# Kernel optimization log

Measured on AMD Instinct MI355X. Metric: run time of the kernel, lower is better.

Reference implementation:

```python
import jax, jax.numpy as jnp
import numpy as np

# fixed 9 neighborhood offsets (center + 8 directions), in pixel units
BASE = np.array([[0,0],[-1,-1],[0,-1],[1,-1],[-1,0],[1,0],[-1,1],[0,1],[1,1]], dtype=np.float32)
MAX_DELTA = 0.5 / 512.0


def bilinear_sample(vm, gx, gy):
    """vm: (D,H,W); gx,gy: (N,) normalized grid coords in [-1,1].
    Bilinear, padding_mode='zeros', align_corners=True. Returns (D,N)."""
    D, H, W = vm.shape
    ix = (gx + 1.0) * 0.5 * (W - 1)
    iy = (gy + 1.0) * 0.5 * (H - 1)
    x0 = jnp.floor(ix); y0 = jnp.floor(iy)
    x1 = x0 + 1.0;      y1 = y0 + 1.0
    wx1 = ix - x0; wx0 = 1.0 - wx1
    wy1 = iy - y0; wy0 = 1.0 - wy1
    fm = vm.reshape(D, H * W)

    def corner(xf, yf, wx, wy):
        valid = (xf >= 0) & (xf <= W - 1) & (yf >= 0) & (yf <= H - 1)
        xi = jnp.clip(xf.astype(jnp.int32), 0, W - 1)
        yi = jnp.clip(yf.astype(jnp.int32), 0, H - 1)
        v = jnp.take(fm, yi * W + xi, axis=1)  # (D,N) gather
        w = jnp.where(valid, wx * wy, 0.0)
        return v * w

    return (corner(x0, y0, wx0, wy0) + corner(x1, y0, wx1, wy0)
            + corner(x0, y1, wx0, wy1) + corner(x1, y1, wx1, wy1))


def setup_inputs() -> dict:
    key = jax.random.key(0)
    ks = jax.random.split(key, 5)
    B, C, Hf, Wf = 4, 256, 128, 128
    T, D = 16384, 128
    fmap = jax.random.normal(ks[0], (B, C, Hf, Wf), dtype=jnp.float32)
    coords = jax.random.uniform(ks[1], (B, T, 2), dtype=jnp.float32)
    W_proj = jax.random.normal(ks[2], (D, C), dtype=jnp.float32) * (1.0 / np.sqrt(C))
    W1 = jax.random.normal(ks[3], (D, D), dtype=jnp.float32) * (1.0 / np.sqrt(D))
    b1 = jnp.zeros((D,), dtype=jnp.float32)
    W2 = jax.random.normal(ks[4], (2, D), dtype=jnp.float32) * (1.0 / np.sqrt(D))
    b2 = jnp.zeros((2,), dtype=jnp.float32)
    return {"fmap": fmap, "coords": coords, "W_proj": W_proj,
            "W1": W1, "b1": b1, "W2": W2, "b2": b2}


def reference(fmap, coords, W_proj, W1, b1, W2, b2):
    B, C, Hf, Wf = fmap.shape
    T = coords.shape[1]
    K = BASE.shape[0]
    # 1x1 conv projection
    vm = jnp.einsum('bchw,dc->bdhw', fmap, W_proj)  # (B,D,Hf,Wf)
    # offsets: one pixel step in [0,1] coords (align_corners=True)
    step = jnp.array([1.0 / (Wf - 1), 1.0 / (Hf - 1)], dtype=coords.dtype)
    grid = coords[:, :, None, :] + jnp.asarray(BASE)[None, None] * step  # (B,T,K,2)
    grid = grid * 2.0 - 1.0                                            # normalize to [-1,1]
    grid = grid.reshape(B, T * K, 2)
    feat = jax.vmap(bilinear_sample)(vm, grid[..., 0], grid[..., 1])   # (B,D,T*K)
    D = feat.shape[1]
    feat = feat.transpose(0, 2, 1).reshape(B, T, K, D).mean(axis=2)    # (B,T,D)
    h = jax.nn.relu(feat @ W1.T + b1)
    delta = jnp.tanh(h @ W2.T + b2) * MAX_DELTA
    return coords + delta
```

## Files before the change

kernel.cpp:

```cpp
#include <hip/hip_runtime.h>
#include <cstddef>

#define NB 4
#define NC 256
#define ND 128
#define NH 128
#define NW 128
#define NHW (NH*NW)
#define NT 16384
#define NBKT 1024
#define CAP 192
#define FS 136
#define GGRID 3072
#define CSTRIDE 16

typedef short   short8  __attribute__((ext_vector_type(8)));
typedef unsigned short ushort8 __attribute__((ext_vector_type(8)));
typedef float   floatx4 __attribute__((ext_vector_type(4)));
typedef float   floatx2 __attribute__((ext_vector_type(2)));

__device__ __forceinline__ unsigned pk_bf16(float a, float b) {
    unsigned ua = __float_as_uint(a);
    unsigned ub = __float_as_uint(b);
    ua += 0x7fffu + ((ua >> 16) & 1u);
    ub += 0x7fffu + ((ub >> 16) & 1u);
    return (ua >> 16) | (ub & 0xffff0000u);
}

__device__ __forceinline__ unsigned fp8x4_from_f32(float v0, float v1, float v2, float v3) {
    int r = 0;
    r = __builtin_amdgcn_cvt_pk_fp8_f32(v0, v1, r, false);
    r = __builtin_amdgcn_cvt_pk_fp8_f32(v2, v3, r, true);
    return (unsigned)r;
}
template <bool HI>
__device__ __forceinline__ floatx2 fp8x2_to_f32(unsigned w) {
    return __builtin_amdgcn_cvt_pk_f32_fp8((int)w, HI);
}

__device__ __forceinline__ int bucket_of(float cx, float cy, int b) {
    int x0 = (int)floorf(cx * (float)(NW - 1));
    int y0 = (int)floorf(cy * (float)(NH - 1));
    x0 = min(max(x0, 0), NW - 1);
    y0 = min(max(y0, 0), NH - 1);
    return b * 256 + (y0 >> 3) * 16 + (x0 >> 3);
}

__global__ __launch_bounds__(512, 4)
void proj_fused(const float* __restrict__ fmap, const float* __restrict__ coords,
                const float* __restrict__ Wp, const float* __restrict__ W1,
                int* __restrict__ counts, int* __restrict__ order,
                unsigned short* __restrict__ W1bf, unsigned char* __restrict__ vm)
{
    const int bi = blockIdx.x;
    const int t  = threadIdx.x;

    if (t < 128) {
        const int g = bi * 128 + t;
        const float cx = coords[(size_t)g*2 + 0];
        const float cy = coords[(size_t)g*2 + 1];
        const int bkt = bucket_of(cx, cy, g >> 14);
        const int pos = atomicAdd(&counts[bkt*CSTRIDE], 1);
        if (pos < CAP) order[bkt*CAP + pos] = g;
    } else if (t < 160) {
        const int i = bi * 32 + (t - 128);
        unsigned u = __float_as_uint(W1[i]);
        u += 0x7fffu + ((u >> 16) & 1u);
        W1bf[i] = (unsigned short)(u >> 16);
    }

    __shared__ unsigned short awp[8*8*64*8];
    __shared__ float ftile[32*128];

    const int lane = t & 63;
    const int w    = t >> 6;
    const int l15  = lane & 15;
    const int q    = lane >> 4;
    const int cq   = q * 8;

    {
        const int dt = w;
        const float* wr0 = Wp + (size_t)(dt*16 + l15)*NC + cq;
        #pragma unroll
        for (int ch = 0; ch < 8; ++ch) {
            float4 g0 = *(const float4*)(wr0 + ch*32);
            float4 g1 = *(const float4*)(wr0 + ch*32 + 4);
            uint4 pk = make_uint4(pk_bf16(g0.x,g0.y), pk_bf16(g0.z,g0.w),
                                  pk_bf16(g1.x,g1.y), pk_bf16(g1.z,g1.w));
            *(uint4*)&awp[((dt*8 + ch)*64 + lane)*8] = pk;
        }
    }

    const int b    = (bi & 7) >> 1;
    const int slot = ((bi >> 3) << 1) | (bi & 1);
    const int pl   = w*16 + l15;

    const int row_thr = t >> 5;
    const int px_off  = (t & 31) * 4;
    const float* gstage = fmap + (size_t)b*NC*NHW + slot*128 + px_off;
    char* ftile_b = (char*)ftile;
    const unsigned wbase = (unsigned)((t >> 6) * 1024);

    floatx4 acc[8];
    #pragma unroll
    for (int i = 0; i < 8; ++i) acc[i] = (floatx4)(0.f);

    #pragma unroll 1
    for (int c0 = 0; c0 < 8; ++c0) {
        __syncthreads();
        {
            const float* g0 = gstage + (size_t)(c0*32 + row_thr)*NHW;
            const float* g1 = g0 + (size_t)16*NHW;
            __builtin_amdgcn_global_load_lds(
                (const __attribute__((address_space(1))) unsigned*)g0,
                (__attribute__((address_space(3))) unsigned*)(ftile_b + wbase), 16, 0, 0);
            __builtin_amdgcn_global_load_lds(
                (const __attribute__((address_space(1))) unsigned*)g1,
                (__attribute__((address_space(3))) unsigned*)(ftile_b + 8192 + wbase), 16, 0, 0);
        }
        __syncthreads();

        union { short8 v; unsigned u[4]; } bc;
        #pragma unroll
        for (int j = 0; j < 4; ++j)
            bc.u[j] = pk_bf16(ftile[(cq + 2*j    )*128 + pl],
                              ftile[(cq + 2*j + 1)*128 + pl]);
        #pragma unroll
        for (int dt = 0; dt < 8; ++dt) {
            short8 afr = *(const short8*)&awp[((dt*8 + c0)*64 + lane)*8];
            acc[dt] = __builtin_amdgcn_mfma_f32_16x16x32_bf16(afr, bc.v, acc[dt], 0, 0, 0);
        }
    }

    __syncthreads();
    {
        unsigned* lw = (unsigned*)ftile;
        const int sw = (pl & 7) << 2;
        #pragma unroll
        for (int dt = 0; dt < 8; ++dt) {
            floatx4 v = acc[dt];
            lw[pl*32 + ((dt*4 + q) ^ sw)] = fp8x4_from_f32(v[0], v[1], v[2], v[3]);
        }
    }
    __syncthreads();
    {
        unsigned char* vmbase = vm + ((size_t)(b*NHW + slot*128))*ND;
        const unsigned* lr = (const unsigned*)ftile;
        #pragma unroll
        for (int k = 0; k < 2; ++k) {
            const int px  = (t >> 3) + k*64;
            const int w8b = (t & 7) * 4;
            uint4 vv = *(const uint4*)&lr[px*32 + (w8b ^ ((px & 7) << 2))];
            *(uint4*)(vmbase + k*8192 + t*16) = vv;
        }
    }
}

__global__ __launch_bounds__(512, 4)
void gather_mlp(const unsigned char* __restrict__ vm, const float* __restrict__ coords,
                const int* __restrict__ counts, const int* __restrict__ order,
                const unsigned short* __restrict__ W1bf, const float* __restrict__ b1,
                const float* __restrict__ W2, const float* __restrict__ b2,
                float* __restrict__ out)
{
    __shared__ unsigned short feat[64 * FS];
    __shared__ float part[64][8];
    __shared__ float W2s[256];
    __shared__ float b1s[128];
    __shared__ int gidx[64];

    const int bkt = blockIdx.x & 1023;
    const int c   = blockIdx.x >> 10;
    const int n   = min(counts[bkt*CSTRIDE], CAP);
    const int np  = min(n - c*64, 64);
    if (np <= 0) return;
    const int t   = threadIdx.x;

    if (t < 128) {
        W2s[t*2]   = W2[t];
        W2s[t*2+1] = W2[ND + t];
        b1s[t]     = b1[t];
    }

    {
        const int pt = t >> 3;
        const int c8 = t & 7;
        if (pt < np) {
            const int g = order[bkt*CAP + c*64 + pt];
            if (c8 == 0) gidx[pt] = g;
            const int b = g >> 14;
            const float cx = coords[(size_t)g*2 + 0];
            const float cy = coords[(size_t)g*2 + 1];
            const float ix = cx * (float)(NW - 1);
            const float iy = cy * (float)(NH - 1);
            const float x0f = floorf(ix), y0f = floorf(iy);
            const int x0 = (int)x0f, y0 = (int)y0f;
            const float wx1 = ix - x0f, wy1 = iy - y0f;
            const float wxv[4] = {1.f - wx1, 1.f, 1.f, wx1};
            const float wyv[4] = {1.f - wy1, 1.f, 1.f, wy1};
            floatx2 acc[8];
            #pragma unroll
            for (int k = 0; k < 8; ++k) acc[k] = (floatx2)(0.f);
            const unsigned char* vmb = vm + (size_t)b*NHW*ND + c8*16;
            #pragma unroll
            for (int j = 0; j < 4; ++j) {
                const int Y  = y0 - 1 + j;
                const int Yc = min(max(Y, 0), NH-1);
                const bool vy = (Y >= 0) & (Y < NH);
                #pragma unroll
                for (int i = 0; i < 4; ++i) {
                    const int X  = x0 - 1 + i;
                    const int Xc = min(max(X, 0), NW-1);
                    const bool vx = (X >= 0) & (X < NW);
                    const float wgt = (vx & vy) ? wxv[i]*wyv[j] : 0.f;
                    uint4 u = *(const uint4*)(vmb + (size_t)(Yc*NW + Xc)*ND);
                    const floatx2 w2 = {wgt, wgt};
                    acc[0] += w2 * fp8x2_to_f32<false>(u.x);
                    acc[1] += w2 * fp8x2_to_f32<true >(u.x);
                    acc[2] += w2 * fp8x2_to_f32<false>(u.y);
                    acc[3] += w2 * fp8x2_to_f32<true >(u.y);
                    acc[4] += w2 * fp8x2_to_f32<false>(u.z);
                    acc[5] += w2 * fp8x2_to_f32<true >(u.z);
                    acc[6] += w2 * fp8x2_to_f32<false>(u.w);
                    acc[7] += w2 * fp8x2_to_f32<true >(u.w);
                }
            }
            const float s9 = 1.f/9.f;
            unsigned pk[8];
            #pragma unroll
            for (int k = 0; k < 8; ++k)
                pk[k] = pk_bf16(acc[k].x*s9, acc[k].y*s9);
            *(uint4*)&feat[pt*FS + c8*16]     = make_uint4(pk[0],pk[1],pk[2],pk[3]);
            *(uint4*)&feat[pt*FS + c8*16 + 8] = make_uint4(pk[4],pk[5],pk[6],pk[7]);
        }
    }
    __syncthreads();

    {
        const int lane = t & 63;
        const int w    = t >> 6;
        const int l15  = lane & 15;
        const int q    = lane >> 4;
        const int mp   = w & 3;
        const int npr  = w >> 2;

        if (npr*32 < np) {
            floatx4 C[2][2];
            #pragma unroll
            for (int mi = 0; mi < 2; ++mi)
                #pragma unroll
                for (int ni = 0; ni < 2; ++ni) C[mi][ni] = (floatx4)(0.f);

            #pragma unroll
            for (int kk = 0; kk < 4; ++kk) {
                short8 a0 = *(const short8*)&W1bf[((mp*2+0)*16 + l15)*ND + kk*32 + q*8];
                short8 a1 = *(const short8*)&W1bf[((mp*2+1)*16 + l15)*ND + kk*32 + q*8];
                short8 f0 = *(const short8*)&feat[((npr*2+0)*16 + l15)*FS + kk*32 + q*8];
                short8 f1 = *(const short8*)&feat[((npr*2+1)*16 + l15)*FS + kk*32 + q*8];
                C[0][0] = __builtin_amdgcn_mfma_f32_16x16x32_bf16(a0, f0, C[0][0], 0, 0, 0);
                C[0][1] = __builtin_amdgcn_mfma_f32_16x16x32_bf16(a0, f1, C[0][1], 0, 0, 0);
                C[1][0] = __builtin_amdgcn_mfma_f32_16x16x32_bf16(a1, f0, C[1][0], 0, 0, 0);
                C[1][1] = __builtin_amdgcn_mfma_f32_16x16x32_bf16(a1, f1, C[1][1], 0, 0, 0);
            }
            #pragma unroll
            for (int ni = 0; ni < 2; ++ni) {
                float s0 = 0.f, s1 = 0.f;
                #pragma unroll
                for (int mi = 0; mi < 2; ++mi) {
                    const int e0 = (mp*2 + mi)*16 + q*4;
                    float4 bq = *(const float4*)&b1s[e0];
                    floatx4 h4 = C[mi][ni];
                    #pragma unroll
                    for (int r = 0; r < 4; ++r) {
                        float hv = fmaxf(h4[r] + (&bq.x)[r], 0.f);
                        float2 wv = *(const float2*)&W2s[(e0 + r)*2];
                        s0 = fmaf(hv, wv.x, s0);
                        s1 = fmaf(hv, wv.y, s1);
                    }
                }
                s0 += __shfl_xor(s0, 16); s0 += __shfl_xor(s0, 32);
                s1 += __shfl_xor(s1, 16); s1 += __shfl_xor(s1, 32);
                if (q == 0) {
                    const int pt = (npr*2 + ni)*16 + l15;
                    part[pt][mp*2 + 0] = s0;
                    part[pt][mp*2 + 1] = s1;
                }
            }
        }
    }
    __syncthreads();

    if (t < np) {
        const int g = gidx[t];
        float s0 = part[t][0] + part[t][2] + part[t][4] + part[t][6];
        float s1 = part[t][1] + part[t][3] + part[t][5] + part[t][7];
        const float cx = coords[(size_t)g*2 + 0];
        const float cy = coords[(size_t)g*2 + 1];
        const float MD = 0.5f / 512.0f;
        float2 o = make_float2(cx + tanhf(s0 + b2[0]) * MD,
                               cy + tanhf(s1 + b2[1]) * MD);
        *(float2*)&out[(size_t)g*2] = o;
    }
}

extern "C" void kernel_launch(void* const* d_in, const int* in_sizes, int n_in,
                              void* d_out, int out_size, void* d_ws, size_t ws_size,
                              hipStream_t stream)
{
    const float* fmap   = (const float*)d_in[0];
    const float* coords = (const float*)d_in[1];
    const float* Wp     = (const float*)d_in[2];
    const float* W1     = (const float*)d_in[3];
    const float* b1     = (const float*)d_in[4];
    const float* W2     = (const float*)d_in[5];
    const float* b2     = (const float*)d_in[6];
    float* out = (float*)d_out;

    unsigned char* vm = (unsigned char*)d_ws;
    char* base = (char*)d_ws + (size_t)NB*NHW*ND;
    unsigned short* W1bf = (unsigned short*)base;
    int* counts = (int*)(base + 32768);
    int* order  = (int*)(base + 32768 + 65536);

    hipMemsetAsync(counts, 0, NBKT*CSTRIDE*sizeof(int), stream);
    proj_fused<<<dim3(512),   512, 0, stream>>>(fmap, coords, Wp, W1,
                                                counts, order, W1bf, vm);
    gather_mlp<<<dim3(GGRID), 512, 0, stream>>>(vm, coords, counts, order,
                                                W1bf, b1, W2, b2, out);
}
```

Measured before the change: 135.8 us.

## Double-buffer fmap tile loads into LDS in projection kernel

Splits the fmap staging tile into two LDS buffers and prefetches the next channel chunk with global_load_lds while the MFMA work runs on the current one. Explicit vmcnt waits and raw s_barrier calls replace the two __syncthreads per iteration, and the channel loop is fully unrolled. The goal is to hide global load latency in the projection. In exchange LDS use doubles and launch_bounds drops from 4 to 2 blocks per CU, which may reduce occupancy. The hand-written waitcnt and barrier placement carries ordering risk around the wait for the current buffer, especially for the prologue's waves.

```diff
diff --git a/kernel.cpp b/kernel.cpp
--- a/kernel.cpp
+++ b/kernel.cpp
@@ -46,7 +46,7 @@
     return b * 256 + (y0 >> 3) * 16 + (x0 >> 3);
 }
 
-__global__ __launch_bounds__(512, 4)
+__global__ __launch_bounds__(512, 2)
 void proj_fused(const float* __restrict__ fmap, const float* __restrict__ coords,
                 const float* __restrict__ Wp, const float* __restrict__ W1,
                 int* __restrict__ counts, int* __restrict__ order,
@@ -70,7 +70,7 @@
     }
 
     __shared__ unsigned short awp[8*8*64*8];
-    __shared__ float ftile[32*128];
+    __shared__ float ftile[2][32*128];
 
     const int lane = t & 63;
     const int w    = t >> 6;
@@ -105,34 +105,51 @@
     #pragma unroll
     for (int i = 0; i < 8; ++i) acc[i] = (floatx4)(0.f);
 
-    #pragma unroll 1
+    __syncthreads();
+
+    {
+        const float* g0 = gstage + (size_t)(0*32 + row_thr)*NHW;
+        __builtin_amdgcn_global_load_lds(
+            (const __attribute__((address_space(1))) unsigned*)g0,
+            (__attribute__((address_space(3))) unsigned*)(ftile_b + wbase), 16, 0, 0);
+        __builtin_amdgcn_global_load_lds(
+            (const __attribute__((address_space(1))) unsigned*)(g0 + (size_t)16*NHW),
+            (__attribute__((address_space(3))) unsigned*)(ftile_b + 8192 + wbase), 16, 0, 0);
+    }
+
+    #pragma unroll
     for (int c0 = 0; c0 < 8; ++c0) {
-        __syncthreads();
-        {
-            const float* g0 = gstage + (size_t)(c0*32 + row_thr)*NHW;
-            const float* g1 = g0 + (size_t)16*NHW;
+        if (c0 < 7) {
+            const unsigned nb = (unsigned)(((c0+1) & 1) * 16384);
+            const float* g0 = gstage + (size_t)((c0+1)*32 + row_thr)*NHW;
             __builtin_amdgcn_global_load_lds(
                 (const __attribute__((address_space(1))) unsigned*)g0,
-                (__attribute__((address_space(3))) unsigned*)(ftile_b + wbase), 16, 0, 0);
+                (__attribute__((address_space(3))) unsigned*)(ftile_b + nb + wbase), 16, 0, 0);
             __builtin_amdgcn_global_load_lds(
-                (const __attribute__((address_space(1))) unsigned*)g1,
-                (__attribute__((address_space(3))) unsigned*)(ftile_b + 8192 + wbase), 16, 0, 0);
-        }
-        __syncthreads();
-
+                (const __attribute__((address_space(1))) unsigned*)(g0 + (size_t)16*NHW),
+                (__attribute__((address_space(3))) unsigned*)(ftile_b + nb + 8192 + wbase), 16, 0, 0);
+            asm volatile("s_waitcnt vmcnt(2)" ::: "memory");
+        } else {
+            asm volatile("s_waitcnt vmcnt(0)" ::: "memory");
+        }
+        __builtin_amdgcn_sched_barrier(0);
+        __builtin_amdgcn_s_barrier();
+        __builtin_amdgcn_sched_barrier(0);
+
+        const float* ft = ftile[c0 & 1];
         union { short8 v; unsigned u[4]; } bc;
         #pragma unroll
         for (int j = 0; j < 4; ++j)
-            bc.u[j] = pk_bf16(ftile[(cq + 2*j    )*128 + pl],
-                              ftile[(cq + 2*j + 1)*128 + pl]);
+            bc.u[j] = pk_bf16(ft[(cq + 2*j    )*128 + pl],
+                              ft[(cq + 2*j + 1)*128 + pl]);
         #pragma unroll
         for (int dt = 0; dt < 8; ++dt) {
             short8 afr = *(const short8*)&awp[((dt*8 + c0)*64 + lane)*8];
             acc[dt] = __builtin_amdgcn_mfma_f32_16x16x32_bf16(afr, bc.v, acc[dt], 0, 0, 0);
         }
-    }
-
-    __syncthreads();
+        __builtin_amdgcn_s_barrier();
+    }
+
     {
         unsigned* lw = (unsigned*)ftile;
         const int sw = (pl & 7) << 2;
```

After: 138.9 us. 2.3% more time.
